# Kernel tuning notes

Hardware: AMD Instinct MI355X
Metric: run time of the kernel (lower is better)

The kernel has to match this reference:

```python
import jax, jax.numpy as jnp
import numpy as np

TAU = 2.0      # LIF membrane time constant
EPS = 1e-5     # BatchNorm eps
HEADS = 8
SCALE = 0.125
ALPHA = 4.0    # surrogate sigmoid sharpness

@jax.custom_vjp
def spike(x):
    return (x >= 0.0).astype(x.dtype)

def _spike_fwd(x):
    return spike(x), x

def _spike_bwd(x, g):
    s = jax.nn.sigmoid(ALPHA * x)
    return (g * ALPHA * s * (1.0 - s),)

spike.defvjp(_spike_fwd, _spike_bwd)

def lif(x_seq, v_th):
    # multi-step LIF, v_reset=0, hard reset; x_seq: [T, ...]
    def step(v, x):
        v = v + (x - v) / TAU
        s = spike(v - v_th)
        v = (1.0 - s) * v  # hard reset to 0
        return v, s
    v0 = jnp.zeros_like(x_seq[0])
    _, spikes = jax.lax.scan(step, v0, x_seq)
    return spikes

def bn(x, gamma, beta, mean, var):
    # inference-mode BatchNorm1d over channel axis; x: [T,B,C,N], params: [C]
    inv = gamma * jax.lax.rsqrt(var + EPS)
    return x * inv[:, None] + (beta - mean * inv)[:, None]

def setup_inputs() -> dict:
    key = jax.random.key(0)
    k1, k2 = jax.random.split(key)
    T, B, C, N, H = 4, 64, 512, 196, HEADS
    x = jax.random.normal(k1, (T, B, C, N), dtype=jnp.float32)
    res_attn = jnp.zeros((T, B, H, N, N), dtype=jnp.float32)
    w = jax.random.normal(k2, (4, C, C), dtype=jnp.float32) / np.sqrt(C)
    bn_gamma = jnp.ones((4, C), dtype=jnp.float32)
    bn_beta = jnp.zeros((4, C), dtype=jnp.float32)
    bn_mean = jnp.zeros((4, C), dtype=jnp.float32)
    bn_var = jnp.ones((4, C), dtype=jnp.float32)
    return {"x": x, "res_attn": res_attn, "w": w, "bn_gamma": bn_gamma,
            "bn_beta": bn_beta, "bn_mean": bn_mean, "bn_var": bn_var}

def reference(x, res_attn, w, bn_gamma, bn_beta, bn_mean, bn_var):
    T, B, C, N = x.shape
    H = HEADS
    D = C // H

    def qkv_branch(i):
        y = jnp.einsum('oc,tbcn->tbon', w[i], x)          # conv1x1
        y = bn(y, bn_gamma[i], bn_beta[i], bn_mean[i], bn_var[i])
        return lif(y, 1.0)                                # binary spikes

    def to_heads(t):  # [T,B,C,N] -> [T,B,H,N,D]
        return t.transpose(0, 1, 3, 2).reshape(T, B, N, H, D).transpose(0, 1, 3, 2, 4)

    q = to_heads(qkv_branch(0))
    k = to_heads(qkv_branch(1))
    v = to_heads(qkv_branch(2))

    attn = jnp.einsum('tbhnd,tbhmd->tbhnm', q, k) * SCALE
    o = jnp.einsum('tbhnm,tbhmd->tbhnd', attn, v)
    o = o.transpose(0, 1, 2, 4, 3).reshape(T, B, C, N)    # [T,B,H,D,N] -> [T,B,C,N]
    o = lif(o, 0.5)                                       # attn_lif, v_threshold=0.5
    o = jnp.einsum('oc,tbcn->tbon', w[3], o)              # proj conv1x1
    o = bn(o, bn_gamma[3], bn_beta[3], bn_mean[3], bn_var[3])
    o = lif(o, 1.0)                                       # proj_lif
    return (o, attn)
```

## Files before the change

### kernel.cpp

```cpp
#include <hip/hip_runtime.h>
#include <stdint.h>
#include <math.h>

#define T_ 4
#define B_ 64
#define C_ 512
#define N_ 196
#define H_ 8
#define OE_ 25690112ull
#define TBHN (T_*B_*H_*N_)

using u16 = unsigned short;
using u32 = unsigned int;
using u64 = unsigned long long;
using u8  = unsigned char;

typedef __attribute__((ext_vector_type(8))) short bf16x8;
typedef __attribute__((ext_vector_type(4))) float f32x4;
typedef const float __attribute__((address_space(4))) cfloat_as4;

typedef const void __attribute__((address_space(1))) gvoid;
typedef void __attribute__((address_space(3))) svoid;

__device__ __forceinline__ void gld_lds4(const void* g, void* l){
  __builtin_amdgcn_global_load_lds((gvoid*)g, (svoid*)l, 4, 0, 0);
}

__device__ __forceinline__ float b2f(u16 u){
  union { u32 i; float f; } x; x.i = ((u32)u) << 16; return x.f;
}
__device__ __forceinline__ u16 f2b(float f){
  union { float g; u32 i; } x; x.g = f; return (u16)(x.i >> 16);
}
__device__ __forceinline__ float ldf(const void* p, size_t i, bool f32){
  return f32 ? ((const float*)p)[i] : b2f(((const u16*)p)[i]);
}
__device__ __forceinline__ bool is_f32(const void* var){
  return ((const u32*)var)[0] == 0x3F800000u;
}

__global__ __launch_bounds__(256) void transpose_w(
    const void* __restrict__ w, float* __restrict__ wT, const void* __restrict__ var)
{
  const bool f32 = is_f32(var);
  __shared__ float tile[32][33];
  const int br = blockIdx.z;
  const int c0 = blockIdx.x*32, o0 = blockIdx.y*32;
  const int tx = threadIdx.x & 31, ty = threadIdx.x >> 5;
  const size_t base = (size_t)br*C_*C_;
  #pragma unroll
  for (int r = 0; r < 32; r += 8)
    tile[ty+r][tx] = ldf(w, base + (size_t)(o0+ty+r)*C_ + (c0+tx), f32);
  __syncthreads();
  #pragma unroll
  for (int r = 0; r < 32; r += 8)
    wT[base + (size_t)(c0+ty+r)*C_ + (o0+tx)] = tile[tx][ty+r];
}

template<int DT>
__device__ __forceinline__ void conv_main(
    const void* __restrict__ xin, const float* __restrict__ wp,
    u8* __restrict__ xsraw, const int wv, const int lane, const int fl0,
    float acc[4][8])
{
  const size_t cn   = (size_t)C_*N_;
  const size_t tstr = (size_t)B_*cn;

  int e0;
  if (DT == 0)      e0 = lane;
  else if (DT == 1) e0 = 2*(lane & 31);
  else              e0 = 4*(lane & 15);
  const int fl = fl0 + e0;
  const int b  = fl / N_;
  const int n  = fl - b*N_;
  const size_t lbase = (size_t)wv*tstr + (size_t)b*cn + (size_t)n;

  auto issue = [&](int k){
    const int buf = k & 1;
    const int rb  = (buf*4 + wv)*8;
    if (DT == 2){
      const u8* bp = (const u8*)xin + lbase;
      #pragma unroll
      for (int g = 0; g < 2; g++){
        const int cl = g*4 + (lane >> 4);
        gld_lds4(bp + (size_t)(k*8 + cl)*N_, xsraw + (size_t)(rb + g*4)*64);
      }
    } else if (DT == 0){
      const float* bp = (const float*)xin + lbase;
      #pragma unroll
      for (int cl = 0; cl < 8; cl++){
        gld_lds4(bp + (size_t)(k*8 + cl)*N_, xsraw + (size_t)(rb + cl)*256);
      }
    } else {
      const u16* bp = (const u16*)xin + lbase;
      #pragma unroll
      for (int p = 0; p < 4; p++){
        const int cl = p*2 + (lane >> 5);
        gld_lds4(bp + (size_t)(k*8 + cl)*N_, xsraw + (size_t)(rb + p*2)*128);
      }
    }
  };

  issue(0);
  for (int k = 0; k < 64; k++){
    __syncthreads();
    if (k + 1 < 64) issue(k + 1);
    const int buf = k & 1;
    #pragma unroll
    for (int cc = 0; cc < 8; cc++){
      const int c = (k << 3) + cc;
      float xv[4];
      #pragma unroll
      for (int t = 0; t < 4; t++){
        const int ei = ((buf*4 + t)*8 + cc)*64 + lane;
        if (DT == 2)      xv[t] = (float)xsraw[ei];
        else if (DT == 0) xv[t] = ((const float*)xsraw)[ei];
        else              xv[t] = b2f(((const u16*)xsraw)[ei]);
      }
      cfloat_as4* wr = (cfloat_as4*)(uintptr_t)(wp + (size_t)c*C_);
      #pragma unroll
      for (int j = 0; j < 8; j++){
        const float ww = wr[j];
        #pragma unroll
        for (int t = 0; t < 4; t++) acc[t][j] = fmaf(ww, xv[t], acc[t][j]);
      }
    }
  }
}

__global__ __launch_bounds__(256, 6) void conv_qkv(
    const void* __restrict__ xin, const float* __restrict__ wT,
    const void* __restrict__ gamma, const void* __restrict__ beta,
    const void* __restrict__ mean,  const void* __restrict__ var,
    u32* __restrict__ q32, u32* __restrict__ k32, u8* __restrict__ svp)
{
  __shared__ __align__(16) u8 xsraw[16384];
  __shared__ u32 P[256];
  const bool f32 = is_f32(var);
  const int tid  = threadIdx.x;
  const int lane = tid & 63;
  const int wv   = tid >> 6;
  const int cb   = blockIdx.x;
  const int br   = blockIdx.z;
  const int co0  = __builtin_amdgcn_readfirstlane(cb*32 + wv*8);
  const int fl0  = blockIdx.y*64;
  const int fl   = fl0 + lane;
  const int b    = fl / N_;
  const int n    = fl - b*N_;

  if (br < 2){ P[tid] = 0; }

  float acc[4][8];
  #pragma unroll
  for (int t=0;t<4;t++)
    #pragma unroll
    for (int j=0;j<8;j++) acc[t][j] = 0.f;

  const float* __restrict__ wp = wT + (size_t)br*C_*C_ + co0;

  if (f32) conv_main<0>(xin, wp, xsraw, wv, lane, fl0, acc);
  else     conv_main<1>(xin, wp, xsraw, wv, lane, fl0, acc);

  {
    #pragma clang fp contract(off)
    u32 m8[4] = {0,0,0,0};
    #pragma unroll
    for (int j=0;j<8;j++){
      const int co = co0 + j;
      const size_t pb = (size_t)br*C_ + co;
      const float gf  = ldf(gamma, pb, f32);
      const float bef = ldf(beta,  pb, f32);
      const float mnf = ldf(mean,  pb, f32);
      const float vrf = ldf(var,   pb, f32);
      const float rs   = 1.0f / sqrtf(vrf + 1e-5f);
      const float invf = gf * rs;
      const float mi   = mnf * invf;
      const float shf  = bef - mi;
      float vm = 0.f;
      #pragma unroll
      for (int t=0;t<4;t++){
        float xy = acc[t][j] * invf;
        float x  = xy + shf;
        float d  = x - vm;
        float v  = vm + d * 0.5f;
        bool  s  = (v >= 1.0f);
        vm = s ? 0.f : v;
        if (br == 2){
          svp[((size_t)(t*B_ + b)*C_ + co)*(size_t)N_ + n] = s ? 1 : 0;
        } else {
          m8[t] |= (s ? 1u : 0u) << j;
        }
      }
    }
    if (br < 2){
      #pragma unroll
      for (int t=0;t<4;t++)
        atomicOr(&P[t*64 + lane], m8[t] << (wv*8));
    }
  }
  if (br < 2){
    __syncthreads();
    const int t2 = tid >> 6, l2 = tid & 63;
    const int f2 = fl0 + l2;
    const int b2 = f2 / N_, n2 = f2 - b2*N_;
    const int h2 = cb >> 1, half = cb & 1;
    u32* dst = (br == 0) ? q32 : k32;
    dst[(((size_t)(t2*B_ + b2)*H_ + h2)*(size_t)N_ + n2)*2 + half] = P[tid];
  }
}

__global__ __launch_bounds__(256, 6) void conv_proj(
    const void* __restrict__ xin, const float* __restrict__ wT,
    const void* __restrict__ gamma, const void* __restrict__ beta,
    const void* __restrict__ mean,  const void* __restrict__ var,
    void* __restrict__ outp)
{
  __shared__ __align__(16) u8 xsraw[16384];
  const bool f32 = is_f32(var);
  const int tid  = threadIdx.x;
  const int lane = tid & 63;
  const int wv   = tid >> 6;
  const int cb   = blockIdx.x;
  const int co0  = __builtin_amdgcn_readfirstlane(cb*32 + wv*8);
  const int fl0  = blockIdx.y*64;
  const int fl   = fl0 + lane;
  const int b    = fl / N_;
  const int n    = fl - b*N_;

  float acc[4][8];
  #pragma unroll
  for (int t=0;t<4;t++)
    #pragma unroll
    for (int j=0;j<8;j++) acc[t][j] = 0.f;

  const float* __restrict__ wp = wT + (size_t)3*C_*C_ + co0;

  conv_main<2>(xin, wp, xsraw, wv, lane, fl0, acc);

  {
    #pragma clang fp contract(off)
    #pragma unroll
    for (int j=0;j<8;j++){
      const int co = co0 + j;
      const size_t pb = (size_t)3*C_ + co;
      const float gf  = ldf(gamma, pb, f32);
      const float bef = ldf(beta,  pb, f32);
      const float mnf = ldf(mean,  pb, f32);
      const float vrf = ldf(var,   pb, f32);
      const float rs   = 1.0f / sqrtf(vrf + 1e-5f);
      const float invf = gf * rs;
      const float mi   = mnf * invf;
      const float shf  = bef - mi;
      float vm = 0.f;
      #pragma unroll
      for (int t=0;t<4;t++){
        float xy = acc[t][j] * invf;
        float x  = xy + shf;
        float d  = x - vm;
        float v  = vm + d * 0.5f;
        bool  s  = (v >= 1.0f);
        vm = s ? 0.f : v;
        size_t off = ((size_t)(t*B_ + b)*C_ + co)*(size_t)N_ + n;
        if (f32) ((float*)outp)[off] = s ? 1.f : 0.f;
        else     ((u16*)outp)[off]   = s ? (u16)0x3F80 : (u16)0;
      }
    }
  }
}

__global__ __launch_bounds__(256) void attnqk_mfma(
    const u64* __restrict__ q64, const u64* __restrict__ k64,
    void* __restrict__ outp ,
    const u8* __restrict__ sv, u8* __restrict__ s3,
    const void* __restrict__ var)
{
  const bool f32 = is_f32(var);
  __shared__ __align__(16) u8  Vu[64*232];
  __shared__ __align__(16) u16 At[2][16*232];
  const int bx  = blockIdx.x;
  const int gy  = blockIdx.y;
  const int h   = gy & 7, b = gy >> 3;
  const int tid = threadIdx.x;
  const int lane = tid & 63;
  const int mrow = lane & 15, quad = lane >> 4;
  const int d0  = (tid >> 6) * 16;
  float vmem[2][4] = {{0.f,0.f,0.f,0.f},{0.f,0.f,0.f,0.f}};

  for (int t = 0; t < 4; t++){
    const size_t tb  = (size_t)t*B_ + b;
    const size_t tbh = tb*H_ + h;
    __syncthreads();
    {
      const u32* vb = (const u32*)(sv + (tb*C_ + (size_t)h*64)*(size_t)N_);
      #pragma unroll
      for (int it = 0; it < 15; it++){
        int i = it*256 + tid;
        if (i < 64*58){
          int r = i / 58, wd = i - r*58;
          u32 v = (wd < 49) ? vb[r*49 + wd] : 0u;
          *(u32*)(Vu + r*232 + wd*4) = v;
        }
      }
    }
    {
      const u64* kr = k64 + tbh*(size_t)N_;
      const u64* qr = q64 + tbh*(size_t)N_;
      const size_t abase = OE_ + tbh*(size_t)(N_*N_);
      #pragma unroll
      for (int sub = 0; sub < 2; sub++){
        const int n0 = (bx*2 + sub)*16;
        #pragma unroll
        for (int it = 0; it < 7; it++){
          int i = it*256 + tid;
          int r = i / 112, mp = i - r*112;
          int n = n0 + r;
          int m0 = mp*2;
          u64 qv = (n < N_) ? qr[n] : 0ull;
          u64 kk0 = (m0 < N_)     ? kr[m0]     : 0ull;
          u64 kk1 = (m0 + 1 < N_) ? kr[m0 + 1] : 0ull;
          float c0 = (float)__popcll(qv & kk0);
          float c1 = (float)__popcll(qv & kk1);
          *(u32*)(&At[sub][r*232 + m0]) = (u32)f2b(c0) | ((u32)f2b(c1) << 16);
          if (n < N_ && m0 < N_){
            size_t e = abase + (size_t)n*N_ + m0;
            if (f32){
              float2 st; st.x = c0*0.125f; st.y = c1*0.125f;
              *(float2*)((float*)outp + e) = st;
            } else {
              *(u32*)((u16*)outp + e) =
                  (u32)f2b(c0*0.125f) | ((u32)f2b(c1*0.125f) << 16);
            }
          }
        }
      }
    }
    __syncthreads();
    #pragma unroll
    for (int sub = 0; sub < 2; sub++){
      const int nt = bx*2 + sub;
      const int n0 = nt*16;
      f32x4 acc = {0.f, 0.f, 0.f, 0.f};
      #pragma unroll
      for (int k = 0; k < 7; k++){
        bf16x8 av = *(const bf16x8*)(&At[sub][mrow*232 + k*32 + quad*8]);
        u64 vx = *(const u64*)(Vu + (d0+mrow)*232 + k*32 + quad*8);
        u32 x0 = (u32)vx, x1 = (u32)(vx >> 32);
        u32 o0 = (x0 & 1u)*0x3F80u         + (x0 & 0x100u)*0x3F8000u;
        u32 o1 = ((x0 >> 16) & 1u)*0x3F80u + ((x0 >> 16) & 0x100u)*0x3F8000u;
        u32 o2 = (x1 & 1u)*0x3F80u         + (x1 & 0x100u)*0x3F8000u;
        u32 o3 = ((x1 >> 16) & 1u)*0x3F80u + ((x1 >> 16) & 0x100u)*0x3F8000u;
        union { u32 w[4]; bf16x8 v; } bu;
        bu.w[0] = o0; bu.w[1] = o1; bu.w[2] = o2; bu.w[3] = o3;
        acc = __builtin_amdgcn_mfma_f32_16x16x32_bf16(av, bu.v, acc, 0, 0, 0);
      }
      {
        #pragma clang fp contract(off)
        u32 pk = 0;
        #pragma unroll
        for (int r = 0; r < 4; r++){
          float o  = acc[r] * 0.125f;
          float dd = o - vmem[sub][r];
          float v  = vmem[sub][r] + dd * 0.5f;
          bool  s  = (v >= 0.5f);
          vmem[sub][r] = s ? 0.f : v;
          pk |= (s ? 1u : 0u) << (8*r);
        }
        const bool wvalid = (nt < 12) || (nt == 12 && quad == 0);
        if (wvalid){
          const int d = d0 + mrow;
          *(u32*)(s3 + (tb*C_ + (size_t)h*64 + d)*(size_t)N_ + n0 + quad*4) = pk;
        }
      }
    }
  }
}

extern "C" void kernel_launch(void* const* d_in, const int* in_sizes, int n_in,
                              void* d_out, int out_size, void* d_ws, size_t ws_size,
                              hipStream_t stream)
{
  (void)in_sizes; (void)n_in; (void)out_size; (void)ws_size;
  const void* x     = d_in[0];
  const void* w     = d_in[2];
  const void* gamma = d_in[3];
  const void* beta  = d_in[4];
  const void* mean  = d_in[5];
  const void* var   = d_in[6];

  u8*  sv  = (u8*)d_ws;
  u8*  s3  = sv + OE_;
  u64* q64 = (u64*)(s3 + OE_);
  u64* k64 = q64 + TBHN;
  float* wT = (float*)(k64 + TBHN);

  transpose_w<<<dim3(16,16,4), 256, 0, stream>>>(w, wT, var);

  conv_qkv<<<dim3(16, 196, 3), 256, 0, stream>>>(x, wT, gamma, beta, mean, var,
                                                 (u32*)q64, (u32*)k64, sv);

  attnqk_mfma<<<dim3(7, B_*H_), 256, 0, stream>>>(q64, k64, d_out, sv, s3, var);

  conv_proj<<<dim3(16, 196), 256, 0, stream>>>((const void*)s3, wT, gamma, beta,
                                               mean, var, d_out);
}
```

Baseline: 2.087 ms.

## Pre-convert input to fp32 and use 16-byte global-to-LDS loads in QKV conv

Adds a kernel that converts x to an fp32 copy in workspace when there is room, so conv_qkv always takes the fp32 path. That path now issues 16-byte global_load_lds transfers covering 4 consecutive positions per lane instead of 4-byte ones, cutting the number of load instructions. Launch-bound occupancy hints for both conv kernels are raised from 6 to 8. The price is an extra full pass over x (about 100MB read and written) plus extra workspace. If x is already fp32 the conversion is a plain copy.

```diff
diff --git a/kernel.cpp b/kernel.cpp
--- a/kernel.cpp
+++ b/kernel.cpp
@@ -25,6 +25,9 @@
 __device__ __forceinline__ void gld_lds4(const void* g, void* l){
   __builtin_amdgcn_global_load_lds((gvoid*)g, (svoid*)l, 4, 0, 0);
 }
+__device__ __forceinline__ void gld_lds16(const void* g, void* l){
+  __builtin_amdgcn_global_load_lds((gvoid*)g, (svoid*)l, 16, 0, 0);
+}
 
 __device__ __forceinline__ float b2f(u16 u){
   union { u32 i; float f; } x; x.i = ((u32)u) << 16; return x.f;
@@ -37,6 +40,22 @@
 }
 __device__ __forceinline__ bool is_f32(const void* var){
   return ((const u32*)var)[0] == 0x3F800000u;
+}
+
+__global__ __launch_bounds__(256) void cvt_x(
+    const void* __restrict__ x, float* __restrict__ xf, const void* __restrict__ var)
+{
+  const bool f32 = is_f32(var);
+  const size_t stride = (size_t)gridDim.x*256*4;
+  for (size_t i = ((size_t)blockIdx.x*256 + threadIdx.x)*4; i < OE_; i += stride){
+    if (f32){
+      *(float4*)(xf + i) = *(const float4*)((const float*)x + i);
+    } else {
+      ushort4 u = *(const ushort4*)((const u16*)x + i);
+      float4 o; o.x = b2f(u.x); o.y = b2f(u.y); o.z = b2f(u.z); o.w = b2f(u.w);
+      *(float4*)(xf + i) = o;
+    }
+  }
 }
 
 __global__ __launch_bounds__(256) void transpose_w(
@@ -67,7 +86,7 @@
   const size_t tstr = (size_t)B_*cn;
 
   int e0;
-  if (DT == 0)      e0 = lane;
+  if (DT == 0)      e0 = 4*(lane & 15);
   else if (DT == 1) e0 = 2*(lane & 31);
   else              e0 = 4*(lane & 15);
   const int fl = fl0 + e0;
@@ -88,8 +107,9 @@
     } else if (DT == 0){
       const float* bp = (const float*)xin + lbase;
       #pragma unroll
-      for (int cl = 0; cl < 8; cl++){
-        gld_lds4(bp + (size_t)(k*8 + cl)*N_, xsraw + (size_t)(rb + cl)*256);
+      for (int g = 0; g < 2; g++){
+        const int cl = g*4 + (lane >> 4);
+        gld_lds16(bp + (size_t)(k*8 + cl)*N_, xsraw + (size_t)(rb + g*4)*256);
       }
     } else {
       const u16* bp = (const u16*)xin + lbase;
@@ -128,8 +148,8 @@
   }
 }
 
-__global__ __launch_bounds__(256, 6) void conv_qkv(
-    const void* __restrict__ xin, const float* __restrict__ wT,
+__global__ __launch_bounds__(256, 8) void conv_qkv(
+    const void* __restrict__ xin, int xf32, const float* __restrict__ wT,
     const void* __restrict__ gamma, const void* __restrict__ beta,
     const void* __restrict__ mean,  const void* __restrict__ var,
     u32* __restrict__ q32, u32* __restrict__ k32, u8* __restrict__ svp)
@@ -158,8 +178,8 @@
 
   const float* __restrict__ wp = wT + (size_t)br*C_*C_ + co0;
 
-  if (f32) conv_main<0>(xin, wp, xsraw, wv, lane, fl0, acc);
-  else     conv_main<1>(xin, wp, xsraw, wv, lane, fl0, acc);
+  if (xf32 || f32) conv_main<0>(xin, wp, xsraw, wv, lane, fl0, acc);
+  else             conv_main<1>(xin, wp, xsraw, wv, lane, fl0, acc);
 
   {
     #pragma clang fp contract(off)
@@ -209,7 +229,7 @@
   }
 }
 
-__global__ __launch_bounds__(256, 6) void conv_proj(
+__global__ __launch_bounds__(256, 8) void conv_proj(
     const void* __restrict__ xin, const float* __restrict__ wT,
     const void* __restrict__ gamma, const void* __restrict__ beta,
     const void* __restrict__ mean,  const void* __restrict__ var,
@@ -379,7 +399,7 @@
                               void* d_out, int out_size, void* d_ws, size_t ws_size,
                               hipStream_t stream)
 {
-  (void)in_sizes; (void)n_in; (void)out_size; (void)ws_size;
+  (void)in_sizes; (void)n_in; (void)out_size;
   const void* x     = d_in[0];
   const void* w     = d_in[2];
   const void* gamma = d_in[3];
@@ -392,10 +412,20 @@
   u64* q64 = (u64*)(s3 + OE_);
   u64* k64 = q64 + TBHN;
   float* wT = (float*)(k64 + TBHN);
+  float* xf = wT + (size_t)4*C_*C_;
+  const size_t need_xf = (size_t)((u8*)(xf + OE_) - (u8*)d_ws);
+  const int use_xf = (ws_size >= need_xf) ? 1 : 0;
 
   transpose_w<<<dim3(16,16,4), 256, 0, stream>>>(w, wT, var);
 
-  conv_qkv<<<dim3(16, 196, 3), 256, 0, stream>>>(x, wT, gamma, beta, mean, var,
+  const void* xq = x;
+  if (use_xf){
+    cvt_x<<<dim3(4096), 256, 0, stream>>>(x, xf, var);
+    xq = (const void*)xf;
+  }
+
+  conv_qkv<<<dim3(16, 196, 3), 256, 0, stream>>>(xq, use_xf, wT, gamma, beta,
+                                                 mean, var,
                                                  (u32*)q64, (u32*)k64, sv);
 
   attnqk_mfma<<<dim3(7, B_*H_), 256, 0, stream>>>(q64, k64, d_out, sv, s3, var);
```

Result: no change. 2.128 ms (+2.0%).
